# Optimization experiments

Hardware: AMD Instinct MI355X
Metric: run time of the kernel (lower is better)

Reference implementation:

```python
import jax, jax.numpy as jnp
import numpy as np

EMB = 16      # importance embedding channels (ch 0 = logit, 1: = cov features)
NSEG = 196    # n_segments (14x14 superpixel grid)
MC = 16       # num_monte_carlo
TEMP = 1.0    # initial Gumbel/RelaxedBernoulli temperature (compute_temperature(0))
JITTER = 1e-3 # numerical_stability_check: diagonal jitter so Cholesky succeeds


def setup_inputs() -> dict:
    key = jax.random.key(0)
    k1, k2, k3 = jax.random.split(key, 3)
    B, C, H, W = 16, 3, 224, 224
    x = jax.random.normal(k1, (B, C, H, W), jnp.float32)
    groups = jax.random.randint(k2, (B, H, W), 0, NSEG, jnp.int32)
    W_conv = jax.random.normal(k3, (EMB, C), jnp.float32) * 0.1
    b_conv = jnp.zeros((EMB,), jnp.float32)
    return {"x": x, "groups": groups, "W_conv": W_conv, "b_conv": b_conv}


def _group_mean(groups, emb):
    # scatter_reduce(mean, include_self=False): per-batch segment mean, 0 for empty groups
    # emb: [B,E,H,W], groups: [B,H,W] -> [B, NSEG, E]
    B, E, H, W = emb.shape
    flat = emb.reshape(B, E, H * W).transpose(0, 2, 1).reshape(B * H * W, E)
    ids = (groups.reshape(B, H * W).astype(jnp.int32)
           + NSEG * jnp.arange(B, dtype=jnp.int32)[:, None]).reshape(-1)
    sums = jax.ops.segment_sum(flat, ids, num_segments=B * NSEG).reshape(B, NSEG, E)
    cnt = jax.ops.segment_sum(jnp.ones((B * H * W,), flat.dtype), ids,
                              num_segments=B * NSEG).reshape(B, NSEG, 1)
    return sums / jnp.maximum(cnt, 1.0)


def reference(x, groups, W_conv, b_conv):
    B, C, H, W = x.shape
    # importance_predictor as 1x1 conv: [B,C,H,W] -> [B,EMB,H,W]
    emb = jnp.einsum('bchw,ec->behw', x, W_conv) + b_conv[None, :, None, None]

    avg = _group_mean(groups, emb)            # [B, NSEG, EMB]
    mu = avg[:, :, 0]                          # [B, NSEG]
    gemb = avg[:, :, 1:]                       # [B, NSEG, EMB-1]
    # groups_emb.mT @ groups_emb (groups_emb is [B, EMB-1, NSEG] in torch)
    sigma = jnp.einsum('bse,bte->bst', gemb, gemb)
    sigma = sigma + JITTER * jnp.eye(NSEG, dtype=sigma.dtype)

    pixel_probs = jax.nn.sigmoid(emb[:, 0])    # [B, H, W]
    group_probs = jax.nn.sigmoid(mu)           # [B, NSEG]

    # MultivariateNormal(mu, sigma).rsample([MC]).movedim(0,-1)
    L = jnp.linalg.cholesky(sigma)             # [B, NSEG, NSEG]
    kg, ku = jax.random.split(jax.random.key(42))
    eps = jax.random.normal(kg, (B, NSEG, MC), x.dtype)
    logits_mc = mu[:, :, None] + jnp.einsum('bst,btm->bsm', L, eps)  # [B,NSEG,MC]

    # RelaxedBernoulli(temp, probs=sigmoid(logits_mc)).rsample()
    u = jax.random.uniform(ku, (B, NSEG, MC), x.dtype, 1e-6, 1.0 - 1e-6)
    logistic = jnp.log(u) - jnp.log1p(-u)
    relaxed = jax.nn.sigmoid((logits_mc + logistic) / TEMP)
    hard = (relaxed > 0.5).astype(relaxed.dtype)
    groups_mcmc = hard + relaxed - jax.lax.stop_gradient(relaxed)  # straight-through

    # groups_to_mask: gather group decision back to every pixel
    gf = groups.reshape(B, H * W).astype(jnp.int32)
    idx = jnp.broadcast_to(gf[:, :, None], (B, H * W, MC))
    mask = jnp.take_along_axis(groups_mcmc, idx, axis=1)           # [B, HW, MC]
    mask = mask.reshape(B, H, W, MC)
    mask = jnp.broadcast_to(mask[:, None], (B, C, H, W, MC))       # expand channels
    return mask, group_probs, pixel_probs, sigma
```

## Files before the change

### kernel.cpp

```cpp
#include <hip/hip_runtime.h>
#include <stdint.h>

#define HW    50176
#define BATCH 16
#define NSEG  196
#define EMB   16
#define MC    16
#define JITTER 0.001f
#define EBLK  14
#define PXB   3584

__host__ __device__ inline void threefry2x32(uint32_t k0, uint32_t k1,
                                             uint32_t x0, uint32_t x1,
                                             uint32_t& o0, uint32_t& o1) {
  uint32_t k2 = k0 ^ k1 ^ 0x1BD11BDAu;
#define TFR(r) { x0 += x1; x1 = (x1 << (r)) | (x1 >> (32 - (r))); x1 ^= x0; }
  x0 += k0; x1 += k1;
  TFR(13) TFR(15) TFR(26) TFR(6)
  x0 += k1; x1 += k2 + 1u;
  TFR(17) TFR(29) TFR(16) TFR(24)
  x0 += k2; x1 += k0 + 2u;
  TFR(13) TFR(15) TFR(26) TFR(6)
  x0 += k0; x1 += k1 + 3u;
  TFR(17) TFR(29) TFR(16) TFR(24)
  x0 += k1; x1 += k2 + 4u;
  TFR(13) TFR(15) TFR(26) TFR(6)
  x0 += k2; x1 += k0 + 5u;
#undef TFR
  o0 = x0; o1 = x1;
}

__device__ inline float erfinv_f32(float x) {
  float w = -log1pf(-x * x);
  float p;
  if (w < 5.0f) {
    w = w - 2.5f;
    p = 2.81022636e-08f;
    p = 3.43273939e-07f + p * w;
    p = -3.5233877e-06f + p * w;
    p = -4.39150654e-06f + p * w;
    p = 0.00021858087f + p * w;
    p = -0.00125372503f + p * w;
    p = -0.00417768164f + p * w;
    p = 0.246640727f + p * w;
    p = 1.50140941f + p * w;
  } else {
    w = sqrtf(w) - 3.0f;
    p = -0.000200214257f;
    p = 0.000100950558f + p * w;
    p = 0.00134934322f + p * w;
    p = -0.00367342844f + p * w;
    p = 0.00573950773f + p * w;
    p = -0.0076224613f + p * w;
    p = 0.00943887047f + p * w;
    p = 1.00167406f + p * w;
    p = 2.83297682f + p * w;
  }
  return p * x;
}

__device__ inline float bits_to_f01(uint32_t bits) {
  uint32_t fb = (bits >> 9) | 0x3F800000u;
  return __uint_as_float(fb) - 1.0f;
}

__global__ __launch_bounds__(256) void emb_kernel(
    const float* __restrict__ x, const int* __restrict__ groups,
    const float* __restrict__ Wc, const float* __restrict__ bc,
    float* __restrict__ partial, float* __restrict__ pixel_probs) {
  __shared__ float lsum[4 * NSEG];
  int b = blockIdx.x / EBLK;
  int blk = blockIdx.x % EBLK;
  int tid = threadIdx.x;
  for (int i = tid; i < 4 * NSEG; i += 256) lsum[i] = 0.0f;
  __syncthreads();
  const float* xb = x + (size_t)b * 3 * HW;
  float w0 = Wc[0], w1 = Wc[1], w2 = Wc[2], b0 = bc[0];
  for (int k = 0; k < PXB / 256; ++k) {
    int p = blk * PXB + k * 256 + tid;
    float x0 = xb[p], x1 = xb[HW + p], x2 = xb[2 * HW + p];
    int g = groups[b * HW + p];
    float e = w0 * x0 + w1 * x1;
    e = e + w2 * x2 + b0;
    pixel_probs[b * HW + p] = 1.0f / (1.0f + expf(-e));
    atomicAdd(&lsum[g], x0);
    atomicAdd(&lsum[NSEG + g], x1);
    atomicAdd(&lsum[2 * NSEG + g], x2);
    atomicAdd(&lsum[3 * NSEG + g], 1.0f);
  }
  __syncthreads();
  float* pb = partial + (size_t)blockIdx.x * (4 * NSEG);
  if (tid < NSEG) {
#pragma unroll
    for (int c = 0; c < 4; ++c) pb[c * NSEG + tid] = lsum[c * NSEG + tid];
  }
}

__global__ __launch_bounds__(256) void stats_kernel(
    const float* __restrict__ partial, const float* __restrict__ Wc,
    const float* __restrict__ bc, float* __restrict__ mu_ws,
    float* __restrict__ group_probs, float* __restrict__ Gc ) {
  int b = blockIdx.x;
  int i = threadIdx.x;
  if (i >= NSEG) return;
  float sx0 = 0.0f, sx1 = 0.0f, sx2 = 0.0f, cn = 0.0f;
  for (int bb = 0; bb < EBLK; ++bb) {
    const float* pb = partial + (size_t)(b * EBLK + bb) * (4 * NSEG);
    sx0 += pb[i]; sx1 += pb[NSEG + i]; sx2 += pb[2 * NSEG + i]; cn += pb[3 * NSEG + i];
  }
  float denom = fmaxf(cn, 1.0f);
#pragma unroll
  for (int j = 0; j < EMB; ++j) {
    float e = Wc[j * 3 + 0] * sx0 + Wc[j * 3 + 1] * sx1;
    e = e + Wc[j * 3 + 2] * sx2 + bc[j] * cn;
    float v = e / denom;
    if (j == 0) {
      mu_ws[b * NSEG + i] = v;
      group_probs[b * NSEG + i] = 1.0f / (1.0f + expf(-v));
    } else {
      Gc[((size_t)b * 15 + (j - 1)) * NSEG + i] = v;
    }
  }
}

__global__ __launch_bounds__(256) void sigma_kernel(
    const float* __restrict__ Gc, float* __restrict__ sigma_out) {
  int b = blockIdx.x / 7;
  int tile = blockIdx.x % 7;
  int tid = threadIdx.x;
  __shared__ float ge[15][NSEG];
  if (tid < NSEG) {
#pragma unroll
    for (int j = 0; j < 15; ++j) ge[j][tid] = Gc[((size_t)b * 15 + j) * NSEG + tid];
  }
  __syncthreads();
  if (tid >= NSEG) return;
  int t = tid;
  float gt[15];
#pragma unroll
  for (int j = 0; j < 15; ++j) gt[j] = ge[j][t];
  for (int r = 0; r < 28; ++r) {
    int s = tile * 28 + r;
    float acc = 0.0f;
#pragma unroll
    for (int j = 0; j < 15; ++j) acc = fmaf(ge[j][s], gt[j], acc);
    if (s == t) acc += JITTER;
    sigma_out[((size_t)b * NSEG + s) * NSEG + t] = acc;
  }
}

__global__ __launch_bounds__(256, 1) void cholmc_kernel(
    const float* __restrict__ Gc, const float* __restrict__ mu,
    uint32_t kg0, uint32_t kg1, uint32_t ku0, uint32_t ku1,
    float* __restrict__ hard) {
  int b = blockIdx.x;
  int tid = threadIdx.x;
  int lane = tid & 63;
  int wave = tid >> 6;
  __shared__ float eps_lds[NSEG * MC];
  __shared__ __align__(16) float piv[2][16];

  for (int t = tid; t < NSEG * MC; t += 256) {
    uint32_t a0, a1;
    threefry2x32(kg0, kg1, 0u, (uint32_t)(b * NSEG * MC + t), a0, a1);
    float f = bits_to_f01(a0 ^ a1);
    const float lo = -0.99999994f;
    float u = fmaxf(lo, f * (1.0f - lo) + lo);
    eps_lds[t] = 1.4142135623730951f * erfinv_f32(u);
  }

  int i = wave * 64 + lane;
  float g[15];
#pragma unroll
  for (int j = 0; j < 15; ++j)
    g[j] = (i < NSEG) ? Gc[((size_t)b * 15 + j) * NSEG + i] : 0.0f;
  float acc[16];
#pragma unroll
  for (int m = 0; m < 16; ++m) acc[m] = 0.0f;
  if (tid == 0) {
#pragma unroll
    for (int j = 0; j < 15; ++j) piv[0][j] = g[j];
    piv[0][15] = 0.0f;
  }
  __syncthreads();

  const float sj = 0.031622776601683794f;
  for (int k = 0; k < NSEG; ++k) {
    const float* pv = piv[k & 1];
    float4 p0 = *(const float4*)(pv);
    float4 p1 = *(const float4*)(pv + 4);
    float4 p2 = *(const float4*)(pv + 8);
    float4 p3 = *(const float4*)(pv + 12);
    float gk[15] = {p0.x, p0.y, p0.z, p0.w, p1.x, p1.y, p1.z, p1.w,
                    p2.x, p2.y, p2.z, p2.w, p3.x, p3.y, p3.z};
    float t0 = fmaf(gk[0], gk[0], JITTER);
    float t1 = gk[1] * gk[1];   float t2 = gk[2] * gk[2];
    float t3 = gk[3] * gk[3];   float t4 = gk[4] * gk[4];
    float t5 = gk[5] * gk[5];   float t6 = gk[6] * gk[6];
    float t7 = gk[7] * gk[7];   float t8 = gk[8] * gk[8];
    float t9 = gk[9] * gk[9];   float t10 = gk[10] * gk[10];
    float t11 = gk[11] * gk[11]; float t12 = gk[12] * gk[12];
    float t13 = gk[13] * gk[13]; float t14 = gk[14] * gk[14];
    float u0 = t0 + t1, u1 = t2 + t3, u2 = t4 + t5, u3 = t6 + t7;
    float u4 = t8 + t9, u5 = t10 + t11, u6 = t12 + t13;
    float v0 = u0 + u1, v1 = u2 + u3, v2 = u4 + u5, v3 = u6 + t14;
    float jn = (v0 + v1) + (v2 + v3);
    float invd = __builtin_amdgcn_rsqf(jn);
    float dd = jn * invd;
    float beta = (invd * invd) * __builtin_amdgcn_rcpf(fmaf(sj, invd, 1.0f));

    int s0 = k >> 6;
    if (wave >= s0) {
      const float4* ep = (const float4*)(eps_lds + k * MC);
      float4 e0 = ep[0], e1 = ep[1], e2 = ep[2], e3 = ep[3];
      float ek[16] = {e0.x, e0.y, e0.z, e0.w, e1.x, e1.y, e1.z, e1.w,
                      e2.x, e2.y, e2.z, e2.w, e3.x, e3.y, e3.z, e3.w};
      float dot = 0.0f;
#pragma unroll
      for (int j = 0; j < 15; ++j) dot = fmaf(g[j], gk[j], dot);
      float w;
      if (wave == s0) {
        int owner = k & 63;
        w = (lane > owner) ? dot * invd : ((lane == owner) ? dd : 0.0f);
      } else {
        w = dot * invd;
      }
#pragma unroll
      for (int m = 0; m < 16; ++m) acc[m] = fmaf(w, ek[m], acc[m]);
      float bd = beta * dot;
#pragma unroll
      for (int j = 0; j < 15; ++j) g[j] = fmaf(-bd, gk[j], g[j]);
      int kn = k + 1;
      if (kn < NSEG && i == kn) {
        float* pw = piv[kn & 1];
#pragma unroll
        for (int j = 0; j < 15; ++j) pw[j] = g[j];
      }
    }
    __syncthreads();
  }

  if (i < NSEG) {
    float mui = mu[b * NSEG + i];
    float4 outv[4];
    float* op = (float*)outv;
#pragma unroll
    for (int m = 0; m < 16; ++m) {
      uint32_t a0, a1;
      threefry2x32(ku0, ku1, 0u, (uint32_t)(b * NSEG * MC + i * MC + m), a0, a1);
      float f = bits_to_f01(a0 ^ a1);
      const float mn = 1e-6f;
      const float mx = (float)(1.0 - 1e-6);
      float uu = fmaxf(mn, f * (mx - mn) + mn);
      float lg = logf(uu) - log1pf(-uu);
      float z = mui + acc[m] + lg;
      op[m] = (z > 0.0f) ? 1.0f : 0.0f;
    }
    float4* hp = (float4*)(hard + ((size_t)b * NSEG + i) * MC);
#pragma unroll
    for (int q = 0; q < 4; ++q) hp[q] = outv[q];
  }
}

__global__ __launch_bounds__(256) void mask_kernel(
    const int* __restrict__ groups, const float* __restrict__ hard,
    float4* __restrict__ out) {
  int f = blockIdx.x * blockDim.x + threadIdx.x;
  if (f >= BATCH * 3 * HW * 4) return;
  int pix = f >> 2;
  int q = f & 3;
  int b = pix / (3 * HW);
  int p = pix % HW;
  int g = groups[b * HW + p];
  out[f] = ((const float4*)hard)[(b * NSEG + g) * 4 + q];
}

extern "C" void kernel_launch(void* const* d_in, const int* in_sizes, int n_in,
                              void* d_out, int out_size, void* d_ws, size_t ws_size,
                              hipStream_t stream) {
  const float* x = (const float*)d_in[0];
  const int* groups = (const int*)d_in[1];
  const float* Wc = (const float*)d_in[2];
  const float* bc = (const float*)d_in[3];

  float* out = (float*)d_out;
  float* mask_out = out;
  float* gp_out = out + 38535168;
  float* pp_out = gp_out + 3136;
  float* sig_out = pp_out + 802816;

  float* ws = (float*)d_ws;
  float* partial = ws;
  float* mu_ws = ws + 175616;
  float* Gc    = ws + 178752;
  float* hard  = ws;

  emb_kernel<<<BATCH * EBLK, 256, 0, stream>>>(x, groups, Wc, bc, partial, pp_out);
  stats_kernel<<<BATCH, 256, 0, stream>>>(partial, Wc, bc, mu_ws, gp_out, Gc);
  sigma_kernel<<<BATCH * 7, 256, 0, stream>>>(Gc, sig_out);

  uint32_t kg0, kg1, ku0, ku1;
  threefry2x32(0u, 42u, 0u, 0u, kg0, kg1);
  threefry2x32(0u, 42u, 0u, 1u, ku0, ku1);

  cholmc_kernel<<<BATCH, 256, 0, stream>>>(Gc, mu_ws, kg0, kg1, ku0, ku1, hard);
  mask_kernel<<<(BATCH * 3 * HW * 4 + 255) / 256, 256, 0, stream>>>(
      groups, hard, (float4*)mask_out);
}
```

Measured before the change: 269.9 us.

## Fuse stats, sigma and Cholesky-MC kernels into one per-batch kernel

Merges the segment-statistics, sigma outer-product and Cholesky/Monte-Carlo kernels into a single kernel with one block per batch. Per-segment embeddings and mu now stay in shared memory instead of going through global workspace, and two kernel launches are removed. In exchange, the sigma computation, which used to run across 112 blocks, now runs on only 16 blocks, each writing a full 196x196 matrix before the serial Cholesky loop starts. That puts the sigma work on the critical path.

```diff
diff --git a/kernel.cpp b/kernel.cpp
--- a/kernel.cpp
+++ b/kernel.cpp
@@ -96,67 +96,18 @@
   }
 }
 
-__global__ __launch_bounds__(256) void stats_kernel(
+__global__ __launch_bounds__(256, 1) void fused_kernel(
     const float* __restrict__ partial, const float* __restrict__ Wc,
-    const float* __restrict__ bc, float* __restrict__ mu_ws,
-    float* __restrict__ group_probs, float* __restrict__ Gc ) {
-  int b = blockIdx.x;
-  int i = threadIdx.x;
-  if (i >= NSEG) return;
-  float sx0 = 0.0f, sx1 = 0.0f, sx2 = 0.0f, cn = 0.0f;
-  for (int bb = 0; bb < EBLK; ++bb) {
-    const float* pb = partial + (size_t)(b * EBLK + bb) * (4 * NSEG);
-    sx0 += pb[i]; sx1 += pb[NSEG + i]; sx2 += pb[2 * NSEG + i]; cn += pb[3 * NSEG + i];
-  }
-  float denom = fmaxf(cn, 1.0f);
-#pragma unroll
-  for (int j = 0; j < EMB; ++j) {
-    float e = Wc[j * 3 + 0] * sx0 + Wc[j * 3 + 1] * sx1;
-    e = e + Wc[j * 3 + 2] * sx2 + bc[j] * cn;
-    float v = e / denom;
-    if (j == 0) {
-      mu_ws[b * NSEG + i] = v;
-      group_probs[b * NSEG + i] = 1.0f / (1.0f + expf(-v));
-    } else {
-      Gc[((size_t)b * 15 + (j - 1)) * NSEG + i] = v;
-    }
-  }
-}
-
-__global__ __launch_bounds__(256) void sigma_kernel(
-    const float* __restrict__ Gc, float* __restrict__ sigma_out) {
-  int b = blockIdx.x / 7;
-  int tile = blockIdx.x % 7;
-  int tid = threadIdx.x;
-  __shared__ float ge[15][NSEG];
-  if (tid < NSEG) {
-#pragma unroll
-    for (int j = 0; j < 15; ++j) ge[j][tid] = Gc[((size_t)b * 15 + j) * NSEG + tid];
-  }
-  __syncthreads();
-  if (tid >= NSEG) return;
-  int t = tid;
-  float gt[15];
-#pragma unroll
-  for (int j = 0; j < 15; ++j) gt[j] = ge[j][t];
-  for (int r = 0; r < 28; ++r) {
-    int s = tile * 28 + r;
-    float acc = 0.0f;
-#pragma unroll
-    for (int j = 0; j < 15; ++j) acc = fmaf(ge[j][s], gt[j], acc);
-    if (s == t) acc += JITTER;
-    sigma_out[((size_t)b * NSEG + s) * NSEG + t] = acc;
-  }
-}
-
-__global__ __launch_bounds__(256, 1) void cholmc_kernel(
-    const float* __restrict__ Gc, const float* __restrict__ mu,
+    const float* __restrict__ bc,
     uint32_t kg0, uint32_t kg1, uint32_t ku0, uint32_t ku1,
+    float* __restrict__ group_probs, float* __restrict__ sigma_out,
     float* __restrict__ hard) {
   int b = blockIdx.x;
   int tid = threadIdx.x;
   int lane = tid & 63;
   int wave = tid >> 6;
+  __shared__ float ge[15][NSEG];
+  __shared__ float mu_l[NSEG];
   __shared__ float eps_lds[NSEG * MC];
   __shared__ __align__(16) float piv[2][16];
 
@@ -169,11 +120,47 @@
     eps_lds[t] = 1.4142135623730951f * erfinv_f32(u);
   }
 
-  int i = wave * 64 + lane;
+  if (tid < NSEG) {
+    float sx0 = 0.0f, sx1 = 0.0f, sx2 = 0.0f, cn = 0.0f;
+    for (int bb = 0; bb < EBLK; ++bb) {
+      const float* pb = partial + (size_t)(b * EBLK + bb) * (4 * NSEG);
+      sx0 += pb[tid]; sx1 += pb[NSEG + tid];
+      sx2 += pb[2 * NSEG + tid]; cn += pb[3 * NSEG + tid];
+    }
+    float denom = fmaxf(cn, 1.0f);
+#pragma unroll
+    for (int j = 0; j < EMB; ++j) {
+      float e = Wc[j * 3 + 0] * sx0 + Wc[j * 3 + 1] * sx1;
+      e = e + Wc[j * 3 + 2] * sx2 + bc[j] * cn;
+      float v = e / denom;
+      if (j == 0) {
+        mu_l[tid] = v;
+        group_probs[b * NSEG + tid] = 1.0f / (1.0f + expf(-v));
+      } else {
+        ge[j - 1][tid] = v;
+      }
+    }
+  }
+  __syncthreads();
+
+  if (tid < NSEG) {
+    int t = tid;
+    float gt[15];
+#pragma unroll
+    for (int j = 0; j < 15; ++j) gt[j] = ge[j][t];
+    for (int s = 0; s < NSEG; ++s) {
+      float a = 0.0f;
+#pragma unroll
+      for (int j = 0; j < 15; ++j) a = fmaf(ge[j][s], gt[j], a);
+      if (s == t) a += JITTER;
+      sigma_out[((size_t)b * NSEG + s) * NSEG + t] = a;
+    }
+  }
+
+  int i = tid;
   float g[15];
 #pragma unroll
-  for (int j = 0; j < 15; ++j)
-    g[j] = (i < NSEG) ? Gc[((size_t)b * 15 + j) * NSEG + i] : 0.0f;
+  for (int j = 0; j < 15; ++j) g[j] = (i < NSEG) ? ge[j][i] : 0.0f;
   float acc[16];
 #pragma unroll
   for (int m = 0; m < 16; ++m) acc[m] = 0.0f;
@@ -241,7 +228,7 @@
   }
 
   if (i < NSEG) {
-    float mui = mu[b * NSEG + i];
+    float mui = mu_l[i];
     float4 outv[4];
     float* op = (float*)outv;
 #pragma unroll
@@ -291,19 +278,16 @@
 
   float* ws = (float*)d_ws;
   float* partial = ws;
-  float* mu_ws = ws + 175616;
-  float* Gc    = ws + 178752;
-  float* hard  = ws;
+  float* hard    = ws + 175616;
 
   emb_kernel<<<BATCH * EBLK, 256, 0, stream>>>(x, groups, Wc, bc, partial, pp_out);
-  stats_kernel<<<BATCH, 256, 0, stream>>>(partial, Wc, bc, mu_ws, gp_out, Gc);
-  sigma_kernel<<<BATCH * 7, 256, 0, stream>>>(Gc, sig_out);
 
   uint32_t kg0, kg1, ku0, ku1;
   threefry2x32(0u, 42u, 0u, 0u, kg0, kg1);
   threefry2x32(0u, 42u, 0u, 1u, ku0, ku1);
 
-  cholmc_kernel<<<BATCH, 256, 0, stream>>>(Gc, mu_ws, kg0, kg1, ku0, ku1, hard);
+  fused_kernel<<<BATCH, 256, 0, stream>>>(partial, Wc, bc, kg0, kg1, ku0, ku1,
+                                          gp_out, sig_out, hard);
   mask_kernel<<<(BATCH * 3 * HW * 4 + 255) / 256, 256, 0, stream>>>(
       groups, hard, (float4*)mask_out);
 }
```

Result: no change. 272.7 us (+1.0%).
